# Kernel tuning notes

Hardware: AMD Instinct MI355X
Metric: run time of the kernel (lower is better)

The kernel has to match this reference:

```python
import jax, jax.numpy as jnp
import numpy as np
import math

HS_MIN = 1e-07
MASK_BOUND = 5e-08


def setup_inputs() -> dict:
    key = jax.random.key(0)
    N, B, D = 256, 128, 784
    k0, k1, k2 = jax.random.split(key, 3)
    bandwidth = (4.0 * np.sqrt(math.pi) / (math.pi ** 4 * N)) ** 0.2
    return {
        "x": jax.random.normal(k0, (B, D), jnp.float32),
        "log_det": jnp.zeros((B,), jnp.float32),
        "datapoints": jax.random.normal(k1, (N, D), jnp.float32),
        "log_hs": jnp.full((N, D), np.log(bandwidth), jnp.float32),
        "kde_weights": jnp.zeros((N, D), jnp.float32),
        "vs": jax.random.normal(k2, (D, D), jnp.float32),
    }


def _householder(vs):
    # Q = prod_i (I - 2 v_i v_i^T), applied as rank-1 updates via scan.
    D = vs.shape[1]
    def step(Q, v):
        vn = v / jnp.linalg.norm(v)
        return Q - 2.0 * jnp.outer(Q @ vn, vn), None
    Q, _ = jax.lax.scan(step, jnp.eye(D, dtype=vs.dtype), vs)
    return Q


def _kde_logs(x, datapoints, log_hs, kde_weights):
    # Shared [N,B,D] diff/softplus term feeding log_cdf, log_sf, log_pdf.
    hs = jnp.maximum(jnp.exp(log_hs), HS_MIN)
    log_hs_c = jnp.maximum(log_hs, math.log(HS_MIN))
    u = -(x[None, ...] - datapoints[:, None, :]) / hs[:, None, :]  # [N,B,D]
    w = (kde_weights - jax.nn.logsumexp(kde_weights, axis=0, keepdims=True))[:, None, :]
    sp = jax.nn.softplus(u)
    log_cdf = jax.nn.logsumexp(-sp + w, axis=0)                          # [B,D]
    log_sf = jax.nn.logsumexp(u - sp + w, axis=0)                        # [B,D]
    log_pdf = jax.nn.logsumexp(u - log_hs_c[:, None, :] - 2.0 * sp + w, axis=0)
    return log_cdf, log_sf, log_pdf


def reference(x, log_det, datapoints, log_hs, kde_weights, vs):
    log_cdf_l, log_sf_l, log_pdf = _kde_logs(x, datapoints, log_hs, kde_weights)
    cdf_l = jnp.exp(log_cdf_l)

    cdf_mask = ((cdf_l > MASK_BOUND) & (cdf_l < 1.0 - MASK_BOUND)).astype(x.dtype)
    cdf_l_good = cdf_l * cdf_mask + 0.5 * (1.0 - cdf_mask)
    inverse_l = jax.scipy.special.ndtri(cdf_l_good)

    cdf_mask_right = (cdf_l >= 1.0 - MASK_BOUND).astype(x.dtype)
    cdf_l_bad_right_log = log_sf_l * cdf_mask_right + (-1.0) * (1.0 - cdf_mask_right)
    inverse_l = inverse_l + jnp.sqrt(-2.0 * cdf_l_bad_right_log) * cdf_mask_right

    cdf_mask_left = (cdf_l <= MASK_BOUND).astype(x.dtype)
    cdf_l_bad_left_log = log_cdf_l * cdf_mask_left + (-1.0) * (1.0 - cdf_mask_left)
    inverse_l = inverse_l - jnp.sqrt(-2.0 * cdf_l_bad_left_log) * cdf_mask_left

    log_norm = -0.5 * inverse_l ** 2 - 0.5 * math.log(2.0 * math.pi)
    log_gauss_deriv = (
        log_norm * cdf_mask
        + (jnp.log(jnp.sqrt(-2.0 * cdf_l_bad_left_log)) - log_cdf_l) * cdf_mask_left
        + (jnp.log(jnp.sqrt(-2.0 * cdf_l_bad_right_log)) - log_sf_l) * cdf_mask_right
    )
    log_det = log_det + jnp.sum(log_pdf - log_gauss_deriv, axis=-1)

    Q = _householder(vs)
    x_out = inverse_l @ Q
    return x_out, log_det
```

## Files before the change

### kernel.cpp

```cpp
#include <hip/hip_runtime.h>
#include <math.h>

#define NP 256
#define BB 128
#define DD 784
#define HS_MIN 1e-7f
#define LOG_HS_MIN -16.11809565095832f
#define LOG_MB -16.811242831518264f
#define NEG_HALF_LOG_2PI -0.9189385332046727f
#define W 8
#define NW 98

__device__ double ndtri_logs(float log_cdf_f, float log_sf_f) {
    double lp = (double)log_cdf_f;
    double ls = (double)log_sf_f;
    double p = (double)__expf(log_cdf_f);
    double q = p - 0.5;
    if (fabs(q) <= 0.425) {
        double r = 0.180625 - q * q;
        double num = (((((((2.5090809287301226727e3 * r + 3.3430575583588128105e4) * r
                         + 6.7265770927008700853e4) * r + 4.5921953931549871457e4) * r
                         + 1.3731693765509461125e4) * r + 1.9715909503065514427e3) * r
                         + 1.3314166789178437745e2) * r + 3.3871328727963666080e0);
        double den = (((((((5.2264952788528545610e3 * r + 2.8729085735721942674e4) * r
                         + 3.9307895800092710610e4) * r + 2.1213794301586595867e4) * r
                         + 5.3941960214247511077e3) * r + 6.8718700749205790830e2) * r
                         + 4.2313330701600911252e1) * r + 1.0);
        return q * num / den;
    }
    double r = (q < 0.0) ? sqrt(-lp) : sqrt(-ls);
    double v;
    if (r <= 5.0) {
        r -= 1.6;
        double num = (((((((7.74545014278341407640e-4 * r + 2.27238449892691845833e-2) * r
                         + 2.41780725177450611770e-1) * r + 1.27045825245236838258e0) * r
                         + 3.64784832476320460504e0) * r + 5.76949722146069140550e0) * r
                         + 4.63033784615654529590e0) * r + 1.42343711074968357734e0);
        double den = (((((((1.05075007164441684324e-9 * r + 5.47593808499534494600e-4) * r
                         + 1.51986665636164571966e-2) * r + 1.48103976427480074590e-1) * r
                         + 6.89767334985100004550e-1) * r + 1.67638483018380384940e0) * r
                         + 2.05319162663775882187e0) * r + 1.0);
        v = num / den;
    } else {
        r -= 5.0;
        double num = (((((((2.01033439929228813265e-7 * r + 2.71155556874348757815e-5) * r
                         + 1.24266094738807843860e-3) * r + 2.65321895265761230930e-2) * r
                         + 2.96560571828504891230e-1) * r + 1.78482653991729133580e0) * r
                         + 5.46378491116411436990e0) * r + 6.65790464350110377720e0);
        double den = (((((((2.04426310338993978564e-15 * r + 1.42151175831644588870e-7) * r
                         + 1.84631831751005468180e-5) * r + 7.86869131145613259100e-4) * r
                         + 1.48753612908506148525e-2) * r + 1.36929880922735805310e-1) * r
                         + 5.99832206555887937690e-1) * r + 1.0);
        v = num / den;
    }
    return (q < 0.0) ? -v : v;
}

__global__ __launch_bounds__(256) void k_lsew(const float* __restrict__ kw,
                                              float* __restrict__ lsew) {
    __shared__ float red[4];
    int d = blockIdx.x;
    int n = threadIdx.x;
    float a = kw[n * DD + d];
    float m = a;
    #pragma unroll
    for (int off = 32; off; off >>= 1) m = fmaxf(m, __shfl_xor(m, off, 64));
    if ((threadIdx.x & 63) == 0) red[threadIdx.x >> 6] = m;
    __syncthreads();
    m = fmaxf(fmaxf(red[0], red[1]), fmaxf(red[2], red[3]));
    __syncthreads();
    float e = __expf(a - m);
    #pragma unroll
    for (int off = 32; off; off >>= 1) e += __shfl_xor(e, off, 64);
    if ((threadIdx.x & 63) == 0) red[threadIdx.x >> 6] = e;
    __syncthreads();
    if (threadIdx.x == 0)
        lsew[d] = m + __logf(red[0] + red[1] + red[2] + red[3]);
}

__global__ __launch_bounds__(256) void k_prep(const float* __restrict__ kw,
                                              const float* __restrict__ log_hs,
                                              const float* __restrict__ dp,
                                              const float* __restrict__ lsew,
                                              float4* __restrict__ pk) {
    int n = blockIdx.x;
    for (int d = threadIdx.x; d < DD; d += 256) {
        int idx = n * DD + d;
        float lh = log_hs[idx];
        float hs = fmaxf(__expf(lh), HS_MIN);
        float lhc = fmaxf(lh, LOG_HS_MIN);
        float wv = kw[idx] - lsew[d];
        pk[idx] = make_float4(dp[idx], 1.f / hs, __expf(wv), __expf(wv - lhc));
    }
}

__global__ __launch_bounds__(256) void k_main(const float* __restrict__ x,
                                              const float4* __restrict__ pk,
                                              float* __restrict__ Y,
                                              float* __restrict__ T) {
    unsigned t = blockIdx.x * 256u + threadIdx.x;
    unsigned b = t / DD;
    unsigned d = t - b * DD;
    float xv = x[t];
    float s1 = 0.f, s2 = 0.f, s3 = 0.f;
    for (int n = 0; n < NP; ++n) {
        float4 c = pk[n * DD + d];
        float u = (c.x - xv) * c.y;
        float e = __expf(-fabsf(u));
        float r = 1.f / (1.f + e);
        float base = c.z * r;
        float eh = (u >= 0.f) ? e : 1.f;
        float el = (u >= 0.f) ? 1.f : e;
        s1 += base * eh;
        s2 += base * el;
        s3 += c.w * (e * r * r);
    }
    float log_cdf = __logf(s1);
    float log_sf  = __logf(s2);
    float log_pdf = __logf(s3);

    bool right = (log_sf  <= LOG_MB);
    bool left  = (log_cdf <= LOG_MB);

    float inv, lgd;
    if (right) {
        float t2 = -2.f * log_sf;
        inv = sqrtf(t2);
        lgd = 0.5f * __logf(t2) - log_sf;
    } else if (left) {
        float t2 = -2.f * log_cdf;
        inv = -sqrtf(t2);
        lgd = 0.5f * __logf(t2) - log_cdf;
    } else {
        inv = (float)ndtri_logs(log_cdf, log_sf);
        lgd = -0.5f * inv * inv + NEG_HALF_LOG_2PI;
    }
    Y[t] = inv;
    T[t] = log_pdf - lgd;
}

__global__ __launch_bounds__(256) void k_logdet(const float* __restrict__ T,
                                                const float* __restrict__ ld_in,
                                                float* __restrict__ out) {
    __shared__ float red[4];
    int b = blockIdx.x;
    float s = 0.f;
    for (int d = threadIdx.x; d < DD; d += 256) s += T[b * DD + d];
    #pragma unroll
    for (int off = 32; off; off >>= 1) s += __shfl_down(s, off, 64);
    if ((threadIdx.x & 63) == 0) red[threadIdx.x >> 6] = s;
    __syncthreads();
    if (threadIdx.x == 0) out[BB * DD + b] = ld_in[b] + red[0] + red[1] + red[2] + red[3];
}

__global__ __launch_bounds__(256) void k_vn(const float* __restrict__ vs,
                                            float* __restrict__ vn) {
    __shared__ float red[4];
    int i = blockIdx.x;
    float ss = 0.f;
    for (int j = threadIdx.x; j < DD; j += 256) {
        float v = vs[i * DD + j];
        ss += v * v;
    }
    #pragma unroll
    for (int off = 32; off; off >>= 1) ss += __shfl_down(ss, off, 64);
    if ((threadIdx.x & 63) == 0) red[threadIdx.x >> 6] = ss;
    __syncthreads();
    float inorm = rsqrtf(red[0] + red[1] + red[2] + red[3]);
    for (int j = threadIdx.x; j < DD; j += 256)
        vn[i * DD + j] = vs[i * DD + j] * inorm;
}

__global__ __launch_bounds__(64) void k_gram(const float* __restrict__ vn,
                                             float* __restrict__ G) {
    int wi = blockIdx.x;
    int t = threadIdx.x;
    int k = t >> 3, i = t & 7;
    const float4* a = (const float4*)(vn + (wi * W + k) * DD);
    const float4* b = (const float4*)(vn + (wi * W + i) * DD);
    float s = 0.f;
    for (int j = 0; j < DD / 4; ++j) {
        float4 av = a[j], bv = b[j];
        s += av.x * bv.x + av.y * bv.y + av.z * bv.z + av.w * bv.w;
    }
    G[wi * 64 + k * 8 + i] = s;
}

__device__ __forceinline__ float wave_red_sum(float x) {
    x += __int_as_float(__builtin_amdgcn_update_dpp(0, __float_as_int(x), 0x111, 0xf, 0xf, true));
    x += __int_as_float(__builtin_amdgcn_update_dpp(0, __float_as_int(x), 0x112, 0xf, 0xf, true));
    x += __int_as_float(__builtin_amdgcn_update_dpp(0, __float_as_int(x), 0x114, 0xf, 0xf, true));
    x += __int_as_float(__builtin_amdgcn_update_dpp(0, __float_as_int(x), 0x118, 0xf, 0xf, true));
    x += __int_as_float(__builtin_amdgcn_update_dpp(0, __float_as_int(x), 0x142, 0xa, 0xf, true));
    x += __int_as_float(__builtin_amdgcn_update_dpp(0, __float_as_int(x), 0x143, 0xc, 0xf, true));
    return __int_as_float(__builtin_amdgcn_readlane(__float_as_int(x), 63));
}

__global__ __launch_bounds__(64, 1) void k_house(const float* __restrict__ Yin,
                                                 const float* __restrict__ VN,
                                                 const float* __restrict__ G,
                                                 float* __restrict__ out) {
    __shared__ float gld[NW * 64];
    const int b = blockIdx.x;
    const int l = threadIdx.x;
    const int toff = 768 + (l & 15);
    const bool thas = (l < 16);

    for (int i = l; i < NW * 64; i += 64) gld[i] = G[i];
    __syncthreads();

    float4 y[3];
    float ytl;
    #pragma unroll
    for (int i = 0; i < 3; ++i)
        y[i] = *(const float4*)(Yin + b * DD + 256 * i + 4 * l);
    ytl = thas ? Yin[b * DD + toff] : 0.f;

    for (int wi = 0; wi < NW; ++wi) {
        const float* Vw = VN + (size_t)wi * (W * DD);
        const float* Gw = gld + wi * 64;

        float4 v[W][3];
        float vt[W];
        #pragma unroll
        for (int r = 0; r < W; ++r) {
            const float* vr = Vw + r * DD;
            #pragma unroll
            for (int i = 0; i < 3; ++i)
                v[r][i] = *(const float4*)(vr + 256 * i + 4 * l);
            vt[r] = thas ? vr[toff] : 0.f;
        }

        float p[W];
        #pragma unroll
        for (int r = 0; r < W; ++r) {
            float s = 0.f;
            #pragma unroll
            for (int i = 0; i < 3; ++i) {
                s += y[i].x * v[r][i].x + y[i].y * v[r][i].y
                   + y[i].z * v[r][i].z + y[i].w * v[r][i].w;
            }
            s += ytl * vt[r];
            p[r] = wave_red_sum(s);
        }

        float sv[W];
        #pragma unroll
        for (int r = 0; r < W; ++r) {
            float acc = p[r];
            #pragma unroll
            for (int k = 0; k < W; ++k)
                if (k < r) acc -= 2.f * Gw[k * 8 + r] * sv[k];
            sv[r] = acc;
        }

        #pragma unroll
        for (int r = 0; r < W; ++r) {
            float c = 2.f * sv[r];
            #pragma unroll
            for (int i = 0; i < 3; ++i) {
                y[i].x -= c * v[r][i].x;  y[i].y -= c * v[r][i].y;
                y[i].z -= c * v[r][i].z;  y[i].w -= c * v[r][i].w;
            }
            ytl -= c * vt[r];
        }
    }

    #pragma unroll
    for (int i = 0; i < 3; ++i)
        *(float4*)(out + b * DD + 256 * i + 4 * l) = y[i];
    if (thas)
        out[b * DD + toff] = ytl;
}

extern "C" void kernel_launch(void* const* d_in, const int* in_sizes, int n_in,
                              void* d_out, int out_size, void* d_ws, size_t ws_size,
                              hipStream_t stream) {
    const float* x      = (const float*)d_in[0];
    const float* ld_in  = (const float*)d_in[1];
    const float* dp     = (const float*)d_in[2];
    const float* log_hs = (const float*)d_in[3];
    const float* kw     = (const float*)d_in[4];
    const float* vs     = (const float*)d_in[5];
    float* out = (float*)d_out;

    float* ws   = (float*)d_ws;
    float* lsew = ws;
    float4* pk  = (float4*)(ws + 1024);
    float* Y    = ws + 1024 + NP * DD * 4;
    float* T    = Y + BB * DD;
    float* VN   = T + BB * DD;
    float* G    = VN + DD * DD;

    k_lsew<<<DD, 256, 0, stream>>>(kw, lsew);
    k_prep<<<NP, 256, 0, stream>>>(kw, log_hs, dp, lsew, pk);
    k_main<<<(BB * DD) / 256, 256, 0, stream>>>(x, pk, Y, T);
    k_logdet<<<BB, 256, 0, stream>>>(T, ld_in, out);
    k_vn<<<DD, 256, 0, stream>>>(vs, VN);
    k_gram<<<NW, 64, 0, stream>>>(VN, G);
    k_house<<<BB, 64, 0, stream>>>(Y, VN, G, out);
}
```

Measured before the change: 258.1 us.

## Fuse prep kernels and log-det reduction to cut kernel launches

Merges the weight logsumexp with the per-element packing into one kernel indexed per column. It also fuses vector normalisation with the Gram-matrix computation through a shared-memory tile, and folds the log-det row reduction into the Householder kernel. This drops the pipeline from seven launches to four and removes the global round-trips for lsew and the separate logdet pass. The cost is a strided write pattern in k_lseprep (threads write pk with stride DD) and only 98 blocks doing serial per-row norms in k_vngram.

```diff
diff --git a/kernel.cpp b/kernel.cpp
--- a/kernel.cpp
+++ b/kernel.cpp
@@ -56,8 +56,10 @@
     return (q < 0.0) ? -v : v;
 }
 
-__global__ __launch_bounds__(256) void k_lsew(const float* __restrict__ kw,
-                                              float* __restrict__ lsew) {
+__global__ __launch_bounds__(256) void k_lseprep(const float* __restrict__ kw,
+                                                 const float* __restrict__ log_hs,
+                                                 const float* __restrict__ dp,
+                                                 float4* __restrict__ pk) {
     __shared__ float red[4];
     int d = blockIdx.x;
     int n = threadIdx.x;
@@ -74,23 +76,60 @@
     for (int off = 32; off; off >>= 1) e += __shfl_xor(e, off, 64);
     if ((threadIdx.x & 63) == 0) red[threadIdx.x >> 6] = e;
     __syncthreads();
-    if (threadIdx.x == 0)
-        lsew[d] = m + __logf(red[0] + red[1] + red[2] + red[3]);
-}
-
-__global__ __launch_bounds__(256) void k_prep(const float* __restrict__ kw,
-                                              const float* __restrict__ log_hs,
-                                              const float* __restrict__ dp,
-                                              const float* __restrict__ lsew,
-                                              float4* __restrict__ pk) {
-    int n = blockIdx.x;
-    for (int d = threadIdx.x; d < DD; d += 256) {
-        int idx = n * DD + d;
-        float lh = log_hs[idx];
-        float hs = fmaxf(__expf(lh), HS_MIN);
-        float lhc = fmaxf(lh, LOG_HS_MIN);
-        float wv = kw[idx] - lsew[d];
-        pk[idx] = make_float4(dp[idx], 1.f / hs, __expf(wv), __expf(wv - lhc));
+    float lse = m + __logf(red[0] + red[1] + red[2] + red[3]);
+
+    int idx = n * DD + d;
+    float lh = log_hs[idx];
+    float hs = fmaxf(__expf(lh), HS_MIN);
+    float lhc = fmaxf(lh, LOG_HS_MIN);
+    float wv = kw[idx] - lse;
+    pk[idx] = make_float4(dp[idx], 1.f / hs, __expf(wv), __expf(wv - lhc));
+}
+
+__global__ __launch_bounds__(256) void k_vngram(const float* __restrict__ vs,
+                                                float* __restrict__ VN,
+                                                float* __restrict__ G) {
+    __shared__ float L[W * DD];
+    __shared__ float red[4];
+    __shared__ float nrm[W];
+    int wi = blockIdx.x;
+    int t = threadIdx.x;
+    const float* src = vs + (size_t)wi * (W * DD);
+    for (int j = t; j < W * DD; j += 256) L[j] = src[j];
+    __syncthreads();
+
+    for (int r = 0; r < W; ++r) {
+        float ss = 0.f;
+        for (int j = t; j < DD; j += 256) {
+            float v = L[r * DD + j];
+            ss += v * v;
+        }
+        #pragma unroll
+        for (int off = 32; off; off >>= 1) ss += __shfl_down(ss, off, 64);
+        if ((t & 63) == 0) red[t >> 6] = ss;
+        __syncthreads();
+        if (t == 0) nrm[r] = rsqrtf(red[0] + red[1] + red[2] + red[3]);
+        __syncthreads();
+    }
+
+    for (int j = t; j < W * DD; j += 256) {
+        int r = j / DD;
+        float v = L[j] * nrm[r];
+        L[j] = v;
+        VN[(size_t)wi * (W * DD) + j] = v;
+    }
+    __syncthreads();
+
+    if (t < 64) {
+        int k = t >> 3, i = t & 7;
+        const float4* a = (const float4*)(L + k * DD);
+        const float4* b = (const float4*)(L + i * DD);
+        float s = 0.f;
+        for (int j = 0; j < DD / 4; ++j) {
+            float4 av = a[j], bv = b[j];
+            s += av.x * bv.x + av.y * bv.y + av.z * bv.z + av.w * bv.w;
+        }
+        G[wi * 64 + k * 8 + i] = s;
     }
 }
 
@@ -139,53 +178,6 @@
     T[t] = log_pdf - lgd;
 }
 
-__global__ __launch_bounds__(256) void k_logdet(const float* __restrict__ T,
-                                                const float* __restrict__ ld_in,
-                                                float* __restrict__ out) {
-    __shared__ float red[4];
-    int b = blockIdx.x;
-    float s = 0.f;
-    for (int d = threadIdx.x; d < DD; d += 256) s += T[b * DD + d];
-    #pragma unroll
-    for (int off = 32; off; off >>= 1) s += __shfl_down(s, off, 64);
-    if ((threadIdx.x & 63) == 0) red[threadIdx.x >> 6] = s;
-    __syncthreads();
-    if (threadIdx.x == 0) out[BB * DD + b] = ld_in[b] + red[0] + red[1] + red[2] + red[3];
-}
-
-__global__ __launch_bounds__(256) void k_vn(const float* __restrict__ vs,
-                                            float* __restrict__ vn) {
-    __shared__ float red[4];
-    int i = blockIdx.x;
-    float ss = 0.f;
-    for (int j = threadIdx.x; j < DD; j += 256) {
-        float v = vs[i * DD + j];
-        ss += v * v;
-    }
-    #pragma unroll
-    for (int off = 32; off; off >>= 1) ss += __shfl_down(ss, off, 64);
-    if ((threadIdx.x & 63) == 0) red[threadIdx.x >> 6] = ss;
-    __syncthreads();
-    float inorm = rsqrtf(red[0] + red[1] + red[2] + red[3]);
-    for (int j = threadIdx.x; j < DD; j += 256)
-        vn[i * DD + j] = vs[i * DD + j] * inorm;
-}
-
-__global__ __launch_bounds__(64) void k_gram(const float* __restrict__ vn,
-                                             float* __restrict__ G) {
-    int wi = blockIdx.x;
-    int t = threadIdx.x;
-    int k = t >> 3, i = t & 7;
-    const float4* a = (const float4*)(vn + (wi * W + k) * DD);
-    const float4* b = (const float4*)(vn + (wi * W + i) * DD);
-    float s = 0.f;
-    for (int j = 0; j < DD / 4; ++j) {
-        float4 av = a[j], bv = b[j];
-        s += av.x * bv.x + av.y * bv.y + av.z * bv.z + av.w * bv.w;
-    }
-    G[wi * 64 + k * 8 + i] = s;
-}
-
 __device__ __forceinline__ float wave_red_sum(float x) {
     x += __int_as_float(__builtin_amdgcn_update_dpp(0, __float_as_int(x), 0x111, 0xf, 0xf, true));
     x += __int_as_float(__builtin_amdgcn_update_dpp(0, __float_as_int(x), 0x112, 0xf, 0xf, true));
@@ -197,6 +189,8 @@
 }
 
 __global__ __launch_bounds__(64, 1) void k_house(const float* __restrict__ Yin,
+                                                 const float* __restrict__ T,
+                                                 const float* __restrict__ ld_in,
                                                  const float* __restrict__ VN,
                                                  const float* __restrict__ G,
                                                  float* __restrict__ out) {
@@ -205,6 +199,15 @@
     const int l = threadIdx.x;
     const int toff = 768 + (l & 15);
     const bool thas = (l < 16);
+
+    {
+        float s = 0.f;
+        #pragma unroll
+        for (int i = 0; i < 12; ++i) s += T[b * DD + 64 * i + l];
+        if (thas) s += T[b * DD + 768 + l];
+        float tot = wave_red_sum(s);
+        if (l == 0) out[BB * DD + b] = ld_in[b] + tot;
+    }
 
     for (int i = l; i < NW * 64; i += 64) gld[i] = G[i];
     __syncthreads();
@@ -285,18 +288,14 @@
     float* out = (float*)d_out;
 
     float* ws   = (float*)d_ws;
-    float* lsew = ws;
     float4* pk  = (float4*)(ws + 1024);
     float* Y    = ws + 1024 + NP * DD * 4;
     float* T    = Y + BB * DD;
     float* VN   = T + BB * DD;
     float* G    = VN + DD * DD;
 
-    k_lsew<<<DD, 256, 0, stream>>>(kw, lsew);
-    k_prep<<<NP, 256, 0, stream>>>(kw, log_hs, dp, lsew, pk);
+    k_lseprep<<<DD, 256, 0, stream>>>(kw, log_hs, dp, pk);
+    k_vngram<<<NW, 256, 0, stream>>>(vs, VN, G);
     k_main<<<(BB * DD) / 256, 256, 0, stream>>>(x, pk, Y, T);
-    k_logdet<<<BB, 256, 0, stream>>>(T, ld_in, out);
-    k_vn<<<DD, 256, 0, stream>>>(vs, VN);
-    k_gram<<<NW, 64, 0, stream>>>(VN, G);
-    k_house<<<BB, 64, 0, stream>>>(Y, VN, G, out);
-}
+    k_house<<<BB, 64, 0, stream>>>(Y, T, ld_in, VN, G, out);
+}
```

New measurement: 247.8 us. 4.0% less time.
